# Kernel tuning notes

Hardware: AMD Instinct MI355X
Metric: run time of the kernel (lower is better)

The kernel has to match this reference:

```python
import jax, jax.numpy as jnp
import numpy as np

B, T, C = 4, 2048, 1024
H = 16
HD = C // H

def setup_inputs() -> dict:
    key = jax.random.key(0)
    k1, k2, k3 = jax.random.split(key, 3)
    hidden_states = jax.random.normal(k1, (B, T, C), dtype=jnp.float32)
    qkv_w = jax.random.normal(k2, (3 * C, C), dtype=jnp.float32) * (C ** -0.5)
    qkv_b = jnp.zeros((3 * C,), dtype=jnp.float32)
    o_w = jax.random.normal(k3, (C, C), dtype=jnp.float32) * (C ** -0.5)
    o_b = jnp.zeros((C,), dtype=jnp.float32)
    return {"hidden_states": hidden_states, "qkv_w": qkv_w, "qkv_b": qkv_b,
            "o_w": o_w, "o_b": o_b}

def reference(hidden_states, qkv_w, qkv_b, o_w, o_b):
    b, t, c = hidden_states.shape
    scaling = HD ** -0.5
    # fused QKV projection (torch Linear: x @ W^T + b)
    qkv = jnp.einsum('btc,dc->btd', hidden_states, qkv_w) + qkv_b
    q, k, v = jnp.split(qkv, 3, axis=-1)
    # [B, H, T, HD]
    q = q.reshape(b, t, H, HD).transpose(0, 2, 1, 3)
    k = k.reshape(b, t, H, HD).transpose(0, 2, 1, 3)
    v = v.reshape(b, t, H, HD).transpose(0, 2, 1, 3)
    attn = jnp.einsum('bhqd,bhkd->bhqk', q, k) * scaling
    causal = jnp.tril(jnp.ones((t, t), dtype=bool))
    attn = jnp.where(causal[None, None], attn, -jnp.inf)
    attn = jax.nn.softmax(attn, axis=-1)
    # dropout: eval mode (identity), matching deterministic reference
    out = jnp.einsum('bhqk,bhkd->bhqd', attn, v)
    out = out.transpose(0, 2, 1, 3).reshape(b, t, c)
    out = jnp.einsum('btc,dc->btd', out, o_w) + o_b
    return out
```

## Files before the change

kernel.cpp:

```cpp
#include <hip/hip_runtime.h>
#include <hip/hip_bf16.h>
#include <stdint.h>

#define TLEN 2048
#define NHEAD 16
#define CD 1024
#define HDIM 64

typedef __attribute__((ext_vector_type(4))) float f32x4;
typedef __attribute__((ext_vector_type(8))) short s16x8;
typedef __attribute__((ext_vector_type(8))) unsigned short u16x8;
typedef __attribute__((ext_vector_type(4))) unsigned short u16x4;
typedef __attribute__((ext_vector_type(2))) unsigned int u32x2;

typedef __attribute__((address_space(1))) const unsigned int global_u32;
typedef __attribute__((address_space(3))) unsigned int lds_u32;

__device__ __forceinline__ void gl_lds16(const void* g, void* l) {
  __builtin_amdgcn_global_load_lds((global_u32*)g, (lds_u32*)l, 16, 0, 0);
}

__device__ __forceinline__ unsigned short f2bf(float x) {
  unsigned int u = __float_as_uint(x);
  u += 0x7fffu + ((u >> 16) & 1u);
  return (unsigned short)(u >> 16);
}

__device__ __forceinline__ f32x4 mfma_bf16(s16x8 a, s16x8 b, f32x4 c) {
  return __builtin_amdgcn_mfma_f32_16x16x32_bf16(a, b, c, 0, 0, 0);
}

__global__ __launch_bounds__(256) void cvt_bf16(const float* __restrict__ src,
                                                unsigned short* __restrict__ dst) {
  int i = (blockIdx.x * 256 + threadIdx.x) * 8;
  float4 a = *(const float4*)(src + i);
  float4 b = *(const float4*)(src + i + 4);
  u16x8 o;
  o[0] = f2bf(a.x); o[1] = f2bf(a.y); o[2] = f2bf(a.z); o[3] = f2bf(a.w);
  o[4] = f2bf(b.x); o[5] = f2bf(b.y); o[6] = f2bf(b.z); o[7] = f2bf(b.w);
  *(u16x8*)(dst + i) = o;
}

#define BM 128
#define BN 128
#define BKG 64

template <int SPLIT>
__global__ __launch_bounds__(256) void gemm_bt(
    const unsigned short* __restrict__ A, const unsigned short* __restrict__ Bw,
    const float* __restrict__ bias, float* __restrict__ Cf,
    unsigned short* __restrict__ qk_out, unsigned short* __restrict__ vt_out,
    int M, int N, int K) {
  __shared__ char lds[(BM + BN) * BKG * 2];
  char* aL = lds;
  char* bL = lds + BM * BKG * 2;
  const int tid = threadIdx.x;
  const int w = tid >> 6, l = tid & 63, l15 = l & 15, l4 = l >> 4;
  const int wr = w >> 1, wc = w & 1;

  const int nbx = gridDim.x;
  const int nwg = nbx * gridDim.y;
  int f = blockIdx.y * nbx + blockIdx.x;
  f = (f & 7) * (nwg >> 3) + (f >> 3);
  const int brow = (f / nbx) * BM, bcol = (f % nbx) * BN;

  f32x4 z4 = {0.f, 0.f, 0.f, 0.f};
  f32x4 acc[4][4];
#pragma unroll
  for (int m = 0; m < 4; ++m)
#pragma unroll
    for (int n = 0; n < 4; ++n) acc[m][n] = z4;

  const unsigned short* Ab = A + (size_t)brow * K;
  const unsigned short* Bb = Bw + (size_t)bcol * K;

  for (int k0 = 0; k0 < K; k0 += BKG) {
    __syncthreads();
#pragma unroll
    for (int i = 0; i < 4; ++i) {
      int ch = i * 256 + tid;
      int r = ch >> 3, c = ch & 7;
      int cs = (c ^ (r & 7)) * 8;
      gl_lds16(Ab + (size_t)r * K + k0 + cs, aL + ch * 16);
      gl_lds16(Bb + (size_t)r * K + k0 + cs, bL + ch * 16);
    }
    __syncthreads();
#pragma unroll
    for (int kk = 0; kk < 2; ++kk) {
      s16x8 af[4], bfr[4];
#pragma unroll
      for (int m = 0; m < 4; ++m) {
        int r = wr * 64 + m * 16 + l15;
        af[m] = *(const s16x8*)(aL + r * (BKG * 2) +
                                ((kk * 64 + l4 * 16) ^ ((r & 7) << 4)));
      }
#pragma unroll
      for (int n = 0; n < 4; ++n) {
        int r = wc * 64 + n * 16 + l15;
        bfr[n] = *(const s16x8*)(bL + r * (BKG * 2) +
                                 ((kk * 64 + l4 * 16) ^ ((r & 7) << 4)));
      }
#pragma unroll
      for (int m = 0; m < 4; ++m)
#pragma unroll
        for (int n = 0; n < 4; ++n) acc[m][n] = mfma_bf16(af[m], bfr[n], acc[m][n]);
    }
  }

#pragma unroll
  for (int m = 0; m < 4; ++m) {
    int row0 = brow + wr * 64 + m * 16 + l4 * 4;
#pragma unroll
    for (int n = 0; n < 4; ++n) {
      int col = bcol + wc * 64 + n * 16 + l15;
      float bs = bias[col];
      if (SPLIT == 0) {
#pragma unroll
        for (int r = 0; r < 4; ++r)
          Cf[(size_t)(row0 + r) * N + col] = acc[m][n][r] + bs;
      } else {
        if (col < 2 * CD) {
#pragma unroll
          for (int r = 0; r < 4; ++r)
            qk_out[(size_t)(row0 + r) * (2 * CD) + col] = f2bf(acc[m][n][r] + bs);
        } else {
          int cc = col - 2 * CD;
          int b_ = row0 >> 11;
          int t = row0 & (TLEN - 1);
          u16x4 pk;
#pragma unroll
          for (int r = 0; r < 4; ++r) pk[r] = f2bf(acc[m][n][r] + bs);
          *(u16x4*)(vt_out + (size_t)(b_ * CD + cc) * TLEN + t) = pk;
        }
      }
    }
  }
}

__global__ __launch_bounds__(256) void attn_fwd(
    const unsigned short* __restrict__ qk,
    const unsigned short* __restrict__ vt,
    unsigned short* __restrict__ ctx) {
  __shared__ char k_lds[2 * 64 * 128];
  __shared__ char v_lds[2 * 64 * 128];
  __shared__ char p_lds[4 * 16 * 128];

  const int fblk = blockIdx.y * 16 + blockIdx.x;
  const int xcd = fblk & 7, g = fblk >> 3;
  const int bh = xcd * 8 + (g & 7);
  const int jp = g >> 3;
  const int b = bh >> 4, h = bh & 15;
  const int tid = threadIdx.x;
  const int w = tid >> 6, l = tid & 63, l15 = l & 15, l4 = l >> 4;

  const unsigned short* Kg = qk + (size_t)b * TLEN * (2 * CD) + CD + h * HDIM;
  const unsigned short* Vg = vt + (size_t)bh * HDIM * TLEN;

  const float SC2 = 0.18033688011112042f;
  char* pw = p_lds + w * 2048;

  const int sw = (l15 & 7) << 4;
  const int c0 = (l4 * 16) ^ sw;
  const int c1 = (64 + l4 * 16) ^ sw;
  const int row128 = l15 * 128;
  const char* prd0 = pw + row128 + c0;
  const char* prd1 = pw + row128 + c1;
  char* pwr0 = pw + row128 + ((0 * 32 + l4 * 8) ^ sw);
  char* pwr1 = pw + row128 + ((1 * 32 + l4 * 8) ^ sw);
  char* pwr2 = pw + row128 + ((2 * 32 + l4 * 8) ^ sw);
  char* pwr3 = pw + row128 + ((3 * 32 + l4 * 8) ^ sw);
  const int ch0 = tid, ch1 = 256 + tid;
  const int ldsoff0 = ch0 * 16, ldsoff1 = ch1 * 16;
  const int r0 = ch0 >> 3, r1 = ch1 >> 3;
  const int cs0 = ((ch0 & 7) ^ (r0 & 7)) * 8;
  const int cs1 = ((ch1 & 7) ^ (r1 & 7)) * 8;
  const int bperm_addr = (l ^ 32) << 2;

  s16x8 onesf;
#pragma unroll
  for (int j = 0; j < 8; ++j) onesf[j] = (short)0x3F80;

  f32x4 z4 = {0.f, 0.f, 0.f, 0.f};

  for (int seg = 0; seg < 2; ++seg) {
    const int qi = seg == 0 ? jp : 31 - jp;
    const int nt = qi + 1;

    const unsigned short* qrow =
        qk + (size_t)(b * TLEN + qi * 64 + w * 16 + l15) * (2 * CD) + h * HDIM;
    s16x8 qf0 = *(const s16x8*)(qrow + l4 * 8);
    s16x8 qf1 = *(const s16x8*)(qrow + 32 + l4 * 8);

    f32x4 acc_o[4];
#pragma unroll
    for (int dc = 0; dc < 4; ++dc) acc_o[dc] = z4;
    f32x4 acc_l = z4;
    float m_r = -3.0e38f;

    const char* gk0 = (const char*)Kg + r0 * 4096 + cs0 * 2;
    const char* gk1 = (const char*)Kg + r1 * 4096 + cs1 * 2;
    const char* gv0 = (const char*)Vg + r0 * 4096 + cs0 * 2;
    const char* gv1 = (const char*)Vg + r1 * 4096 + cs1 * 2;

    __builtin_amdgcn_s_barrier();
    gl_lds16(gk0, k_lds + ldsoff0);
    gl_lds16(gv0, v_lds + ldsoff0);
    gl_lds16(gk1, k_lds + ldsoff1);
    gl_lds16(gv1, v_lds + ldsoff1);
    gk0 += 262144; gk1 += 262144; gv0 += 128; gv1 += 128;
    int cur = 0;

    for (int kt = 0; kt < nt; ++kt) {
      __builtin_amdgcn_s_barrier();
      if (kt + 1 < nt) {
        int nb = (cur ^ 1) << 13;
        gl_lds16(gk0, k_lds + nb + ldsoff0);
        gl_lds16(gv0, v_lds + nb + ldsoff0);
        gl_lds16(gk1, k_lds + nb + ldsoff1);
        gl_lds16(gv1, v_lds + nb + ldsoff1);
        gk0 += 262144; gk1 += 262144; gv0 += 128; gv1 += 128;
        asm volatile("s_waitcnt vmcnt(4)" ::: "memory");
      } else {
        asm volatile("s_waitcnt vmcnt(0)" ::: "memory");
      }
      __builtin_amdgcn_sched_barrier(0);
      __builtin_amdgcn_s_barrier();
      __builtin_amdgcn_sched_barrier(0);

      const int cb = cur << 13;
      const char* ka0 = k_lds + cb + row128 + c0;
      const char* ka1 = k_lds + cb + row128 + c1;
      const char* va0 = v_lds + cb + row128 + c0;
      const char* va1 = v_lds + cb + row128 + c1;

      f32x4 s[4];
      __builtin_amdgcn_s_setprio(1);
#pragma unroll
      for (int n = 0; n < 4; ++n) {
        s16x8 kf0 = *(const s16x8*)(ka0 + n * 2048);
        s16x8 kf1 = *(const s16x8*)(ka1 + n * 2048);
        f32x4 z = z4;
        z = mfma_bf16(kf0, qf0, z);
        z = mfma_bf16(kf1, qf1, z);
        s[n] = z;
      }
      __builtin_amdgcn_s_setprio(0);

      if (kt == qi) {
        int ql = w * 16 + l15;
#pragma unroll
        for (int n = 0; n < 4; ++n)
#pragma unroll
          for (int r = 0; r < 4; ++r)
            if ((n * 16 + l4 * 4 + r) > ql) s[n][r] = -3.0e38f;
      }

      float t0 = fmaxf(fmaxf(s[0][0], s[0][1]), fmaxf(s[0][2], s[0][3]));
      float t1 = fmaxf(fmaxf(s[1][0], s[1][1]), fmaxf(s[1][2], s[1][3]));
      float t2 = fmaxf(fmaxf(s[2][0], s[2][1]), fmaxf(s[2][2], s[2][3]));
      float t3 = fmaxf(fmaxf(s[3][0], s[3][1]), fmaxf(s[3][2], s[3][3]));
      float tm = fmaxf(fmaxf(t0, t1), fmaxf(t2, t3));
      tm = fmaxf(tm, __shfl_xor(tm, 16));
      tm = fmaxf(tm, __int_as_float(__builtin_amdgcn_ds_bpermute(
                         bperm_addr, __float_as_int(tm))));

      if (!__all((tm - m_r) * SC2 <= 8.0f)) {
        float m_n = fmaxf(m_r, tm);
        float corr = __builtin_amdgcn_exp2f((m_r - m_n) * SC2);
        m_r = m_n;
        *(float*)(pw + 256 + l15 * 4) = corr;
        asm volatile("s_waitcnt lgkmcnt(0)" ::: "memory");
        __builtin_amdgcn_sched_barrier(0);
        float corr4[4];
#pragma unroll
        for (int r = 0; r < 4; ++r)
          corr4[r] = *(const float*)(pw + 256 + (l4 * 4 + r) * 4);
#pragma unroll
        for (int r = 0; r < 4; ++r) {
          acc_l[r] *= corr4[r];
#pragma unroll
          for (int dc = 0; dc < 4; ++dc) acc_o[dc][r] *= corr4[r];
        }
      }

      float msc = m_r * SC2;
      {
        float p0 = __builtin_amdgcn_exp2f(fmaf(s[0][0], SC2, -msc));
        float p1 = __builtin_amdgcn_exp2f(fmaf(s[0][1], SC2, -msc));
        float p2 = __builtin_amdgcn_exp2f(fmaf(s[0][2], SC2, -msc));
        float p3 = __builtin_amdgcn_exp2f(fmaf(s[0][3], SC2, -msc));
        u32x2 pr;
        pr[0] = (__float_as_uint(p1) & 0xffff0000u) | (__float_as_uint(p0) >> 16);
        pr[1] = (__float_as_uint(p3) & 0xffff0000u) | (__float_as_uint(p2) >> 16);
        *(u32x2*)pwr0 = pr;
        p0 = __builtin_amdgcn_exp2f(fmaf(s[1][0], SC2, -msc));
        p1 = __builtin_amdgcn_exp2f(fmaf(s[1][1], SC2, -msc));
        p2 = __builtin_amdgcn_exp2f(fmaf(s[1][2], SC2, -msc));
        p3 = __builtin_amdgcn_exp2f(fmaf(s[1][3], SC2, -msc));
        pr[0] = (__float_as_uint(p1) & 0xffff0000u) | (__float_as_uint(p0) >> 16);
        pr[1] = (__float_as_uint(p3) & 0xffff0000u) | (__float_as_uint(p2) >> 16);
        *(u32x2*)pwr1 = pr;
        p0 = __builtin_amdgcn_exp2f(fmaf(s[2][0], SC2, -msc));
        p1 = __builtin_amdgcn_exp2f(fmaf(s[2][1], SC2, -msc));
        p2 = __builtin_amdgcn_exp2f(fmaf(s[2][2], SC2, -msc));
        p3 = __builtin_amdgcn_exp2f(fmaf(s[2][3], SC2, -msc));
        pr[0] = (__float_as_uint(p1) & 0xffff0000u) | (__float_as_uint(p0) >> 16);
        pr[1] = (__float_as_uint(p3) & 0xffff0000u) | (__float_as_uint(p2) >> 16);
        *(u32x2*)pwr2 = pr;
        p0 = __builtin_amdgcn_exp2f(fmaf(s[3][0], SC2, -msc));
        p1 = __builtin_amdgcn_exp2f(fmaf(s[3][1], SC2, -msc));
        p2 = __builtin_amdgcn_exp2f(fmaf(s[3][2], SC2, -msc));
        p3 = __builtin_amdgcn_exp2f(fmaf(s[3][3], SC2, -msc));
        pr[0] = (__float_as_uint(p1) & 0xffff0000u) | (__float_as_uint(p0) >> 16);
        pr[1] = (__float_as_uint(p3) & 0xffff0000u) | (__float_as_uint(p2) >> 16);
        *(u32x2*)pwr3 = pr;
      }

      asm volatile("s_waitcnt lgkmcnt(0)" ::: "memory");
      __builtin_amdgcn_sched_barrier(0);

      __builtin_amdgcn_s_setprio(1);
      {
        s16x8 pf0 = *(const s16x8*)prd0;
        s16x8 pf1 = *(const s16x8*)prd1;
        acc_l = mfma_bf16(pf0, onesf, acc_l);
        acc_l = mfma_bf16(pf1, onesf, acc_l);
#pragma unroll
        for (int dc = 0; dc < 4; ++dc) {
          s16x8 vf0 = *(const s16x8*)(va0 + dc * 2048);
          s16x8 vf1 = *(const s16x8*)(va1 + dc * 2048);
          acc_o[dc] = mfma_bf16(pf0, vf0, acc_o[dc]);
          acc_o[dc] = mfma_bf16(pf1, vf1, acc_o[dc]);
        }
      }
      __builtin_amdgcn_s_setprio(0);
      cur ^= 1;
    }

#pragma unroll
    for (int r = 0; r < 4; ++r) {
      int qg = qi * 64 + w * 16 + l4 * 4 + r;
      float inv = 1.0f / acc_l[r];
      size_t base = (size_t)(b * TLEN + qg) * CD + h * HDIM;
#pragma unroll
      for (int dc = 0; dc < 4; ++dc)
        ctx[base + dc * 16 + l15] = f2bf(acc_o[dc][r] * inv);
    }
  }
}

extern "C" void kernel_launch(void* const* d_in, const int* in_sizes, int n_in,
                              void* d_out, int out_size, void* d_ws, size_t ws_size,
                              hipStream_t stream) {
  const float* X  = (const float*)d_in[0];
  const float* Wq = (const float*)d_in[1];
  const float* bq = (const float*)d_in[2];
  const float* Wo = (const float*)d_in[3];
  const float* bo = (const float*)d_in[4];
  float* out = (float*)d_out;

  char* ws = (char*)d_ws;
  unsigned short* Xb  = (unsigned short*)ws;
  unsigned short* Wqb = (unsigned short*)(ws + 16777216);
  unsigned short* Wob = (unsigned short*)(ws + 23068672);
  unsigned short* QK  = (unsigned short*)(ws + 25165824);
  unsigned short* Vt  = (unsigned short*)(ws + 58720256);
  unsigned short* Ctx = Xb;

  cvt_bf16<<<4096, 256, 0, stream>>>(X, Xb);
  cvt_bf16<<<1536, 256, 0, stream>>>(Wq, Wqb);
  cvt_bf16<<<512, 256, 0, stream>>>(Wo, Wob);

  gemm_bt<1><<<dim3(24, 64), 256, 0, stream>>>(Xb, Wqb, bq, nullptr, QK, Vt,
                                               8192, 3072, 1024);
  attn_fwd<<<dim3(16, 64), 256, 0, stream>>>(QK, Vt, Ctx);
  gemm_bt<0><<<dim3(8, 64), 256, 0, stream>>>(Ctx, Wob, bo, out, nullptr, nullptr,
                                              8192, 1024, 1024);
}
```

Measured before the change: 199.6 us.

## Split attention to one q-tile per block, register-stage V, merge conversions

The attention kernel now launches one block per query tile instead of pairing two tiles per block, with the longest tiles scheduled first to balance the causal workload. V is loaded into registers, written to a single LDS buffer each iteration, and only K stays double-buffered through direct global-to-LDS loads. This reduces LDS use and may raise occupancy, but it adds extra barriers and waits and shortens the overlap of V loads. The three fp32-to-bf16 conversion launches are merged into one kernel to save launch overhead.

```diff
diff --git a/kernel.cpp b/kernel.cpp
--- a/kernel.cpp
+++ b/kernel.cpp
@@ -30,9 +30,18 @@
   return __builtin_amdgcn_mfma_f32_16x16x32_bf16(a, b, c, 0, 0, 0);
 }
 
-__global__ __launch_bounds__(256) void cvt_bf16(const float* __restrict__ src,
-                                                unsigned short* __restrict__ dst) {
-  int i = (blockIdx.x * 256 + threadIdx.x) * 8;
+__global__ __launch_bounds__(256) void cvt_all(
+    const float* __restrict__ X, const float* __restrict__ Wq,
+    const float* __restrict__ Wo, unsigned short* __restrict__ Xb,
+    unsigned short* __restrict__ Wqb, unsigned short* __restrict__ Wob) {
+  int blk = blockIdx.x;
+  const float* src;
+  unsigned short* dst;
+  int base;
+  if (blk < 4096) { src = X;  dst = Xb;  base = blk; }
+  else if (blk < 5632) { src = Wq; dst = Wqb; base = blk - 4096; }
+  else { src = Wo; dst = Wob; base = blk - 5632; }
+  int i = (base * 256 + threadIdx.x) * 8;
   float4 a = *(const float4*)(src + i);
   float4 b = *(const float4*)(src + i + 4);
   u16x8 o;
@@ -142,16 +151,18 @@
     const unsigned short* __restrict__ vt,
     unsigned short* __restrict__ ctx) {
   __shared__ char k_lds[2 * 64 * 128];
-  __shared__ char v_lds[2 * 64 * 128];
+  __shared__ char v_lds[64 * 128];
   __shared__ char p_lds[4 * 16 * 128];
 
-  const int fblk = blockIdx.y * 16 + blockIdx.x;
-  const int xcd = fblk & 7, g = fblk >> 3;
-  const int bh = xcd * 8 + (g & 7);
-  const int jp = g >> 3;
+  const int fblk = blockIdx.y * 32 + blockIdx.x;
+  const int xcd = fblk & 7;
+  const int bhi = (fblk >> 3) & 7;
+  const int qi = 31 - (fblk >> 6);
+  const int bh = xcd * 8 + bhi;
   const int b = bh >> 4, h = bh & 15;
   const int tid = threadIdx.x;
   const int w = tid >> 6, l = tid & 63, l15 = l & 15, l4 = l >> 4;
+  const int nt = qi + 1;
 
   const unsigned short* Kg = qk + (size_t)b * TLEN * (2 * CD) + CD + h * HDIM;
   const unsigned short* Vg = vt + (size_t)bh * HDIM * TLEN;
@@ -182,170 +193,148 @@
 
   f32x4 z4 = {0.f, 0.f, 0.f, 0.f};
 
-  for (int seg = 0; seg < 2; ++seg) {
-    const int qi = seg == 0 ? jp : 31 - jp;
-    const int nt = qi + 1;
-
-    const unsigned short* qrow =
-        qk + (size_t)(b * TLEN + qi * 64 + w * 16 + l15) * (2 * CD) + h * HDIM;
-    s16x8 qf0 = *(const s16x8*)(qrow + l4 * 8);
-    s16x8 qf1 = *(const s16x8*)(qrow + 32 + l4 * 8);
-
-    f32x4 acc_o[4];
-#pragma unroll
-    for (int dc = 0; dc < 4; ++dc) acc_o[dc] = z4;
-    f32x4 acc_l = z4;
-    float m_r = -3.0e38f;
-
-    const char* gk0 = (const char*)Kg + r0 * 4096 + cs0 * 2;
-    const char* gk1 = (const char*)Kg + r1 * 4096 + cs1 * 2;
-    const char* gv0 = (const char*)Vg + r0 * 4096 + cs0 * 2;
-    const char* gv1 = (const char*)Vg + r1 * 4096 + cs1 * 2;
-
+  const unsigned short* qrow =
+      qk + (size_t)(b * TLEN + qi * 64 + w * 16 + l15) * (2 * CD) + h * HDIM;
+  s16x8 qf0 = *(const s16x8*)(qrow + l4 * 8);
+  s16x8 qf1 = *(const s16x8*)(qrow + 32 + l4 * 8);
+
+  f32x4 acc_o[4];
+#pragma unroll
+  for (int dc = 0; dc < 4; ++dc) acc_o[dc] = z4;
+  f32x4 acc_l = z4;
+  float m_r = -3.0e38f;
+
+  const char* gk0 = (const char*)Kg + r0 * 4096 + cs0 * 2;
+  const char* gk1 = (const char*)Kg + r1 * 4096 + cs1 * 2;
+  const char* gv0 = (const char*)Vg + r0 * 4096 + cs0 * 2;
+  const char* gv1 = (const char*)Vg + r1 * 4096 + cs1 * 2;
+
+  gl_lds16(gk0, k_lds + ldsoff0);
+  gl_lds16(gk1, k_lds + ldsoff1);
+  s16x8 vstg0 = *(const s16x8*)gv0;
+  s16x8 vstg1 = *(const s16x8*)gv1;
+  int cur = 0;
+
+  for (int kt = 0; kt < nt; ++kt) {
     __builtin_amdgcn_s_barrier();
-    gl_lds16(gk0, k_lds + ldsoff0);
-    gl_lds16(gv0, v_lds + ldsoff0);
-    gl_lds16(gk1, k_lds + ldsoff1);
-    gl_lds16(gv1, v_lds + ldsoff1);
-    gk0 += 262144; gk1 += 262144; gv0 += 128; gv1 += 128;
-    int cur = 0;
-
-    for (int kt = 0; kt < nt; ++kt) {
-      __builtin_amdgcn_s_barrier();
-      if (kt + 1 < nt) {
-        int nb = (cur ^ 1) << 13;
-        gl_lds16(gk0, k_lds + nb + ldsoff0);
-        gl_lds16(gv0, v_lds + nb + ldsoff0);
-        gl_lds16(gk1, k_lds + nb + ldsoff1);
-        gl_lds16(gv1, v_lds + nb + ldsoff1);
-        gk0 += 262144; gk1 += 262144; gv0 += 128; gv1 += 128;
-        asm volatile("s_waitcnt vmcnt(4)" ::: "memory");
-      } else {
-        asm volatile("s_waitcnt vmcnt(0)" ::: "memory");
-      }
-      __builtin_amdgcn_sched_barrier(0);
-      __builtin_amdgcn_s_barrier();
-      __builtin_amdgcn_sched_barrier(0);
-
-      const int cb = cur << 13;
-      const char* ka0 = k_lds + cb + row128 + c0;
-      const char* ka1 = k_lds + cb + row128 + c1;
-      const char* va0 = v_lds + cb + row128 + c0;
-      const char* va1 = v_lds + cb + row128 + c1;
-
-      f32x4 s[4];
-      __builtin_amdgcn_s_setprio(1);
-#pragma unroll
-      for (int n = 0; n < 4; ++n) {
-        s16x8 kf0 = *(const s16x8*)(ka0 + n * 2048);
-        s16x8 kf1 = *(const s16x8*)(ka1 + n * 2048);
-        f32x4 z = z4;
-        z = mfma_bf16(kf0, qf0, z);
-        z = mfma_bf16(kf1, qf1, z);
-        s[n] = z;
-      }
-      __builtin_amdgcn_s_setprio(0);
-
-      if (kt == qi) {
-        int ql = w * 16 + l15;
-#pragma unroll
-        for (int n = 0; n < 4; ++n)
-#pragma unroll
-          for (int r = 0; r < 4; ++r)
-            if ((n * 16 + l4 * 4 + r) > ql) s[n][r] = -3.0e38f;
-      }
-
-      float t0 = fmaxf(fmaxf(s[0][0], s[0][1]), fmaxf(s[0][2], s[0][3]));
-      float t1 = fmaxf(fmaxf(s[1][0], s[1][1]), fmaxf(s[1][2], s[1][3]));
-      float t2 = fmaxf(fmaxf(s[2][0], s[2][1]), fmaxf(s[2][2], s[2][3]));
-      float t3 = fmaxf(fmaxf(s[3][0], s[3][1]), fmaxf(s[3][2], s[3][3]));
-      float tm = fmaxf(fmaxf(t0, t1), fmaxf(t2, t3));
-      tm = fmaxf(tm, __shfl_xor(tm, 16));
-      tm = fmaxf(tm, __int_as_float(__builtin_amdgcn_ds_bpermute(
-                         bperm_addr, __float_as_int(tm))));
-
-      if (!__all((tm - m_r) * SC2 <= 8.0f)) {
-        float m_n = fmaxf(m_r, tm);
-        float corr = __builtin_amdgcn_exp2f((m_r - m_n) * SC2);
-        m_r = m_n;
-        *(float*)(pw + 256 + l15 * 4) = corr;
-        asm volatile("s_waitcnt lgkmcnt(0)" ::: "memory");
-        __builtin_amdgcn_sched_barrier(0);
-        float corr4[4];
+    __builtin_amdgcn_sched_barrier(0);
+    asm volatile("s_waitcnt vmcnt(0)" ::: "memory");
+    *(s16x8*)(v_lds + ldsoff0) = vstg0;
+    *(s16x8*)(v_lds + ldsoff1) = vstg1;
+    if (kt + 1 < nt) {
+      gk0 += 262144; gk1 += 262144; gv0 += 128; gv1 += 128;
+    }
+    {
+      int nb = (cur ^ 1) << 13;
+      gl_lds16(gk0, k_lds + nb + ldsoff0);
+      gl_lds16(gk1, k_lds + nb + ldsoff1);
+    }
+    asm volatile("s_waitcnt lgkmcnt(0)" ::: "memory");
+    __builtin_amdgcn_sched_barrier(0);
+    __builtin_amdgcn_s_barrier();
+    __builtin_amdgcn_sched_barrier(0);
+
+    const int cb = cur << 13;
+    const char* ka0 = k_lds + cb + row128 + c0;
+    const char* ka1 = k_lds + cb + row128 + c1;
+
+    f32x4 s[4];
+    __builtin_amdgcn_s_setprio(1);
+#pragma unroll
+    for (int n = 0; n < 4; ++n) {
+      s16x8 kf0 = *(const s16x8*)(ka0 + n * 2048);
+      s16x8 kf1 = *(const s16x8*)(ka1 + n * 2048);
+      f32x4 z = z4;
+      z = mfma_bf16(kf0, qf0, z);
+      z = mfma_bf16(kf1, qf1, z);
+      s[n] = z;
+    }
+    __builtin_amdgcn_s_setprio(0);
+
+    if (kt == qi) {
+      int ql = w * 16 + l15;
+#pragma unroll
+      for (int n = 0; n < 4; ++n)
 #pragma unroll
         for (int r = 0; r < 4; ++r)
-          corr4[r] = *(const float*)(pw + 256 + (l4 * 4 + r) * 4);
-#pragma unroll
-        for (int r = 0; r < 4; ++r) {
-          acc_l[r] *= corr4[r];
-#pragma unroll
-          for (int dc = 0; dc < 4; ++dc) acc_o[dc][r] *= corr4[r];
-        }
-      }
-
-      float msc = m_r * SC2;
-      {
-        float p0 = __builtin_amdgcn_exp2f(fmaf(s[0][0], SC2, -msc));
-        float p1 = __builtin_amdgcn_exp2f(fmaf(s[0][1], SC2, -msc));
-        float p2 = __builtin_amdgcn_exp2f(fmaf(s[0][2], SC2, -msc));
-        float p3 = __builtin_amdgcn_exp2f(fmaf(s[0][3], SC2, -msc));
-        u32x2 pr;
-        pr[0] = (__float_as_uint(p1) & 0xffff0000u) | (__float_as_uint(p0) >> 16);
-        pr[1] = (__float_as_uint(p3) & 0xffff0000u) | (__float_as_uint(p2) >> 16);
-        *(u32x2*)pwr0 = pr;
-        p0 = __builtin_amdgcn_exp2f(fmaf(s[1][0], SC2, -msc));
-        p1 = __builtin_amdgcn_exp2f(fmaf(s[1][1], SC2, -msc));
-        p2 = __builtin_amdgcn_exp2f(fmaf(s[1][2], SC2, -msc));
-        p3 = __builtin_amdgcn_exp2f(fmaf(s[1][3], SC2, -msc));
-        pr[0] = (__float_as_uint(p1) & 0xffff0000u) | (__float_as_uint(p0) >> 16);
-        pr[1] = (__float_as_uint(p3) & 0xffff0000u) | (__float_as_uint(p2) >> 16);
-        *(u32x2*)pwr1 = pr;
-        p0 = __builtin_amdgcn_exp2f(fmaf(s[2][0], SC2, -msc));
-        p1 = __builtin_amdgcn_exp2f(fmaf(s[2][1], SC2, -msc));
-        p2 = __builtin_amdgcn_exp2f(fmaf(s[2][2], SC2, -msc));
-        p3 = __builtin_amdgcn_exp2f(fmaf(s[2][3], SC2, -msc));
-        pr[0] = (__float_as_uint(p1) & 0xffff0000u) | (__float_as_uint(p0) >> 16);
-        pr[1] = (__float_as_uint(p3) & 0xffff0000u) | (__float_as_uint(p2) >> 16);
-        *(u32x2*)pwr2 = pr;
-        p0 = __builtin_amdgcn_exp2f(fmaf(s[3][0], SC2, -msc));
-        p1 = __builtin_amdgcn_exp2f(fmaf(s[3][1], SC2, -msc));
-        p2 = __builtin_amdgcn_exp2f(fmaf(s[3][2], SC2, -msc));
-        p3 = __builtin_amdgcn_exp2f(fmaf(s[3][3], SC2, -msc));
-        pr[0] = (__float_as_uint(p1) & 0xffff0000u) | (__float_as_uint(p0) >> 16);
-        pr[1] = (__float_as_uint(p3) & 0xffff0000u) | (__float_as_uint(p2) >> 16);
-        *(u32x2*)pwr3 = pr;
-      }
-
+          if ((n * 16 + l4 * 4 + r) > ql) s[n][r] = -3.0e38f;
+    }
+
+    float t0 = fmaxf(fmaxf(s[0][0], s[0][1]), fmaxf(s[0][2], s[0][3]));
+    float t1 = fmaxf(fmaxf(s[1][0], s[1][1]), fmaxf(s[1][2], s[1][3]));
+    float t2 = fmaxf(fmaxf(s[2][0], s[2][1]), fmaxf(s[2][2], s[2][3]));
+    float t3 = fmaxf(fmaxf(s[3][0], s[3][1]), fmaxf(s[3][2], s[3][3]));
+    float tm = fmaxf(fmaxf(t0, t1), fmaxf(t2, t3));
+    tm = fmaxf(tm, __shfl_xor(tm, 16));
+    tm = fmaxf(tm, __int_as_float(__builtin_amdgcn_ds_bpermute(
+                       bperm_addr, __float_as_int(tm))));
+
+    if (!__all((tm - m_r) * SC2 <= 8.0f)) {
+      float m_n = fmaxf(m_r, tm);
+      float corr = __builtin_amdgcn_exp2f((m_r - m_n) * SC2);
+      m_r = m_n;
+      *(float*)(pw + 256 + l15 * 4) = corr;
       asm volatile("s_waitcnt lgkmcnt(0)" ::: "memory");
       __builtin_amdgcn_sched_barrier(0);
-
-      __builtin_amdgcn_s_setprio(1);
-      {
-        s16x8 pf0 = *(const s16x8*)prd0;
-        s16x8 pf1 = *(const s16x8*)prd1;
-        acc_l = mfma_bf16(pf0, onesf, acc_l);
-        acc_l = mfma_bf16(pf1, onesf, acc_l);
-#pragma unroll
-        for (int dc = 0; dc < 4; ++dc) {
-          s16x8 vf0 = *(const s16x8*)(va0 + dc * 2048);
-          s16x8 vf1 = *(const s16x8*)(va1 + dc * 2048);
-          acc_o[dc] = mfma_bf16(pf0, vf0, acc_o[dc]);
-          acc_o[dc] = mfma_bf16(pf1, vf1, acc_o[dc]);
-        }
-      }
-      __builtin_amdgcn_s_setprio(0);
-      cur ^= 1;
-    }
-
-#pragma unroll
-    for (int r = 0; r < 4; ++r) {
-      int qg = qi * 64 + w * 16 + l4 * 4 + r;
-      float inv = 1.0f / acc_l[r];
-      size_t base = (size_t)(b * TLEN + qg) * CD + h * HDIM;
-#pragma unroll
-      for (int dc = 0; dc < 4; ++dc)
-        ctx[base + dc * 16 + l15] = f2bf(acc_o[dc][r] * inv);
-    }
+      float corr4[4];
+#pragma unroll
+      for (int r = 0; r < 4; ++r)
+        corr4[r] = *(const float*)(pw + 256 + (l4 * 4 + r) * 4);
+#pragma unroll
+      for (int r = 0; r < 4; ++r) {
+        acc_l[r] *= corr4[r];
+#pragma unroll
+        for (int dc = 0; dc < 4; ++dc) acc_o[dc][r] *= corr4[r];
+      }
+    }
+
+    float msc = m_r * SC2;
+#pragma unroll
+    for (int n = 0; n < 4; ++n) {
+      float p0 = __builtin_amdgcn_exp2f(fmaf(s[n][0], SC2, -msc));
+      float p1 = __builtin_amdgcn_exp2f(fmaf(s[n][1], SC2, -msc));
+      float p2 = __builtin_amdgcn_exp2f(fmaf(s[n][2], SC2, -msc));
+      float p3 = __builtin_amdgcn_exp2f(fmaf(s[n][3], SC2, -msc));
+      u32x2 pr;
+      pr[0] = (__float_as_uint(p1) & 0xffff0000u) | (__float_as_uint(p0) >> 16);
+      pr[1] = (__float_as_uint(p3) & 0xffff0000u) | (__float_as_uint(p2) >> 16);
+      char* dst = (n == 0) ? pwr0 : (n == 1) ? pwr1 : (n == 2) ? pwr2 : pwr3;
+      *(u32x2*)dst = pr;
+    }
+
+    asm volatile("s_waitcnt lgkmcnt(0)" ::: "memory");
+    __builtin_amdgcn_sched_barrier(0);
+
+    vstg0 = *(const s16x8*)gv0;
+    vstg1 = *(const s16x8*)gv1;
+    __builtin_amdgcn_sched_barrier(0);
+
+    __builtin_amdgcn_s_setprio(1);
+    {
+      s16x8 pf0 = *(const s16x8*)prd0;
+      s16x8 pf1 = *(const s16x8*)prd1;
+      acc_l = mfma_bf16(pf0, onesf, acc_l);
+      acc_l = mfma_bf16(pf1, onesf, acc_l);
+#pragma unroll
+      for (int dc = 0; dc < 4; ++dc) {
+        s16x8 vf0 = *(const s16x8*)(v_lds + dc * 2048 + row128 + c0);
+        s16x8 vf1 = *(const s16x8*)(v_lds + dc * 2048 + row128 + c1);
+        acc_o[dc] = mfma_bf16(pf0, vf0, acc_o[dc]);
+        acc_o[dc] = mfma_bf16(pf1, vf1, acc_o[dc]);
+      }
+    }
+    __builtin_amdgcn_s_setprio(0);
+    cur ^= 1;
+  }
+
+#pragma unroll
+  for (int r = 0; r < 4; ++r) {
+    int qg = qi * 64 + w * 16 + l4 * 4 + r;
+    float inv = 1.0f / acc_l[r];
+    size_t base = (size_t)(b * TLEN + qg) * CD + h * HDIM;
+#pragma unroll
+    for (int dc = 0; dc < 4; ++dc)
+      ctx[base + dc * 16 + l15] = f2bf(acc_o[dc][r] * inv);
   }
 }
 
@@ -367,13 +356,11 @@
   unsigned short* Vt  = (unsigned short*)(ws + 58720256);
   unsigned short* Ctx = Xb;
 
-  cvt_bf16<<<4096, 256, 0, stream>>>(X, Xb);
-  cvt_bf16<<<1536, 256, 0, stream>>>(Wq, Wqb);
-  cvt_bf16<<<512, 256, 0, stream>>>(Wo, Wob);
+  cvt_all<<<6144, 256, 0, stream>>>(X, Wq, Wo, Xb, Wqb, Wob);
 
   gemm_bt<1><<<dim3(24, 64), 256, 0, stream>>>(Xb, Wqb, bq, nullptr, QK, Vt,
                                                8192, 3072, 1024);
-  attn_fwd<<<dim3(16, 64), 256, 0, stream>>>(QK, Vt, Ctx);
+  attn_fwd<<<dim3(32, 64), 256, 0, stream>>>(QK, Vt, Ctx);
   gemm_bt<0><<<dim3(8, 64), 256, 0, stream>>>(Ctx, Wob, bo, out, nullptr, nullptr,
                                               8192, 1024, 1024);
 }
```

Measured after the change: 173.5 us. 13.0% less time.
